# Kernel tuning notes

Hardware: AMD Instinct MI355X
Metric: run time of the kernel (lower is better)

Reference implementation:

```python
import jax, jax.numpy as jnp
import numpy as np
import math

HIDDEN = 2048
HEADS = 16
HEAD_DIM = HIDDEN // HEADS
RANK = HIDDEN // 2  # rank_ratio=0.5
B, S = 1, 4096


def setup_inputs() -> dict:
    key = jax.random.key(0)
    ks = jax.random.split(key, 10)
    sd = lambda fan_in: 1.0 / math.sqrt(fan_in)
    inp = {
        "hidden_states": jax.random.normal(ks[0], (B, S, HIDDEN), dtype=jnp.float32),
        "attention_mask": jnp.zeros((B, 1, S, S), dtype=jnp.float32),
        # low-rank projection weights; Linear weight shape is [out, in]
        "q_V": jax.random.uniform(ks[1], (RANK, HIDDEN), jnp.float32, -sd(HIDDEN), sd(HIDDEN)),
        "q_U": jax.random.uniform(ks[2], (HIDDEN, RANK), jnp.float32, -sd(RANK), sd(RANK)),
        "k_V": jax.random.uniform(ks[3], (RANK, HIDDEN), jnp.float32, -sd(HIDDEN), sd(HIDDEN)),
        "k_U": jax.random.uniform(ks[4], (HIDDEN, RANK), jnp.float32, -sd(RANK), sd(RANK)),
        "v_V": jax.random.uniform(ks[5], (RANK, HIDDEN), jnp.float32, -sd(HIDDEN), sd(HIDDEN)),
        "v_U": jax.random.uniform(ks[6], (HIDDEN, RANK), jnp.float32, -sd(RANK), sd(RANK)),
        "o_W": jax.random.uniform(ks[7], (HIDDEN, HIDDEN), jnp.float32, -sd(HIDDEN), sd(HIDDEN)),
        "o_b": jax.random.uniform(ks[8], (HIDDEN,), jnp.float32, -sd(HIDDEN), sd(HIDDEN)),
    }
    return inp


def _split_heads(x):
    # [B,S,HIDDEN] -> [B,H,S,Dh]
    b, s, _ = x.shape
    return x.reshape(b, s, HEADS, HEAD_DIM).transpose(0, 2, 1, 3)


def reference(hidden_states, attention_mask, q_V, q_U, k_V, k_U, v_V, v_U, o_W, o_b):
    # low-rank QKV: x @ V^T @ U^T
    q = _split_heads((hidden_states @ q_V.T) @ q_U.T)
    k = _split_heads((hidden_states @ k_V.T) @ k_U.T)
    v = _split_heads((hidden_states @ v_V.T) @ v_U.T)
    scores = jnp.einsum("bhqd,bhkd->bhqk", q, k) / math.sqrt(HEAD_DIM)
    scores = scores + attention_mask
    attn = jax.nn.softmax(scores, axis=-1)
    out = jnp.einsum("bhqk,bhkd->bhqd", attn, v)
    out = out.transpose(0, 2, 1, 3).reshape(hidden_states.shape[0], hidden_states.shape[1], HIDDEN)
    out = out @ o_W.T + o_b
    return out
```

## Files before the change

kernel.cpp:

```cpp
#include <hip/hip_runtime.h>

#define HIDDEN 2048
#define HEADS 16
#define HD 128
#define RANK 1024
#define SEQ 4096

typedef __bf16 bf16_t;
typedef __bf16 bf16x8 __attribute__((ext_vector_type(8)));
typedef __bf16 bf16x4 __attribute__((ext_vector_type(4)));
typedef float f32x4 __attribute__((ext_vector_type(4)));

#define MFMA_BF16(a, b, c) __builtin_amdgcn_mfma_f32_16x16x32_bf16((a), (b), (c), 0, 0, 0)

__device__ __forceinline__ void gload16(const bf16_t* g, bf16_t* l) {
  __builtin_amdgcn_global_load_lds(
      (const __attribute__((address_space(1))) unsigned int*)g,
      (__attribute__((address_space(3))) unsigned int*)l, 16, 0, 0);
}

struct CastSeg { const float* s; bf16_t* d; int n4; };
struct CastArgs { CastSeg seg[8]; };

__global__ __launch_bounds__(256) void cast_bf16_kernel(CastArgs a) {
  const int stride = gridDim.x * blockDim.x;
  const int tid0 = blockIdx.x * blockDim.x + threadIdx.x;
#pragma unroll
  for (int i = 0; i < 8; i++) {
    const float4* src = (const float4*)a.seg[i].s;
    bf16x4* dst = (bf16x4*)a.seg[i].d;
    const int n4 = a.seg[i].n4;
    for (int j = tid0; j < n4; j += stride) {
      float4 v = src[j];
      dst[j] = bf16x4{(bf16_t)v.x, (bf16_t)v.y, (bf16_t)v.z, (bf16_t)v.w};
    }
  }
}

template <int OUT_MODE>
__global__ __launch_bounds__(256) void gemm3(const bf16_t* __restrict__ A, int lda, int aOff,
                                             const bf16_t* __restrict__ W0,
                                             const bf16_t* __restrict__ W1,
                                             const bf16_t* __restrict__ W2,
                                             int nPerThird, int K,
                                             void* __restrict__ Cp, int ldc, size_t cOff,
                                             const float* __restrict__ bias, float s0,
                                             bf16_t* __restrict__ Ct) {
  __shared__ bf16_t As[128 * 32];
  __shared__ bf16_t Bs[128 * 32];
  const int tid = threadIdx.x, lane = tid & 63, wave = tid >> 6;
  const int wr = wave >> 1, wc = wave & 1, quad = lane >> 4, l15 = lane & 15;
  const int n0g = blockIdx.x * 128;
  const int third = n0g / nPerThird;
  const int n0 = n0g - third * nPerThird;
  const bf16_t* W = third == 0 ? W0 : (third == 1 ? W1 : W2);
  const bf16_t* Ab = A + (size_t)third * aOff;
  const int m0 = blockIdx.y * 128;
  const float sc = (third == 0) ? s0 : 1.f;

  f32x4 acc[4][4];
#pragma unroll
  for (int i = 0; i < 4; i++)
#pragma unroll
    for (int j = 0; j < 4; j++) acc[i][j] = f32x4{0.f, 0.f, 0.f, 0.f};

  const int KT = K >> 5;
  for (int kt = 0; kt < KT; ++kt) {
#pragma unroll
    for (int i = 0; i < 2; i++) {
      int slot = (wave * 2 + i) * 64 + lane;
      int row = slot >> 2, cp = slot & 3;
      int cl = cp ^ ((row >> 1) & 3);
      gload16(Ab + (size_t)(m0 + row) * lda + kt * 32 + cl * 8, As + (size_t)(wave * 2 + i) * 512);
    }
#pragma unroll
    for (int i = 0; i < 2; i++) {
      int slot = (wave * 2 + i) * 64 + lane;
      int row = slot >> 2, cp = slot & 3;
      int cl = cp ^ ((row >> 1) & 3);
      gload16(W + (size_t)(n0 + row) * K + kt * 32 + cl * 8, Bs + (size_t)(wave * 2 + i) * 512);
    }
    __syncthreads();

    bf16x8 af[4], bfr[4];
#pragma unroll
    for (int mt = 0; mt < 4; mt++) {
      int row = wr * 64 + mt * 16 + l15;
      int phys = quad ^ ((row >> 1) & 3);
      af[mt] = *reinterpret_cast<const bf16x8*>(As + row * 32 + phys * 8);
    }
#pragma unroll
    for (int nt = 0; nt < 4; nt++) {
      int row = wc * 64 + nt * 16 + l15;
      int phys = quad ^ ((row >> 1) & 3);
      bfr[nt] = *reinterpret_cast<const bf16x8*>(Bs + row * 32 + phys * 8);
    }
#pragma unroll
    for (int mt = 0; mt < 4; mt++)
#pragma unroll
      for (int nt = 0; nt < 4; nt++) acc[mt][nt] = MFMA_BF16(af[mt], bfr[nt], acc[mt][nt]);
    __syncthreads();
  }

  if constexpr (OUT_MODE == 2) {
    if (third == 2) {
#pragma unroll
      for (int nt = 0; nt < 4; nt++) {
        int col = n0 + wc * 64 + nt * 16 + l15;
#pragma unroll
        for (int mt = 0; mt < 4; mt++) {
          int rowb = m0 + wr * 64 + mt * 16 + quad * 4;
          bf16x4 tv = {(bf16_t)acc[mt][nt][0], (bf16_t)acc[mt][nt][1],
                       (bf16_t)acc[mt][nt][2], (bf16_t)acc[mt][nt][3]};
          *reinterpret_cast<bf16x4*>(Ct + (size_t)col * SEQ + rowb) = tv;
        }
      }
      return;
    }
  }

#pragma unroll
  for (int nt = 0; nt < 4; nt++) {
    int col = n0 + wc * 64 + nt * 16 + l15;
    float bv = 0.f;
    if constexpr (OUT_MODE == 1) bv = bias[col];
#pragma unroll
    for (int mt = 0; mt < 4; mt++) {
      int rowb = m0 + wr * 64 + mt * 16 + quad * 4;
#pragma unroll
      for (int r = 0; r < 4; r++) {
        float vx = acc[mt][nt][r];
        if constexpr (OUT_MODE == 1)
          ((float*)Cp + (size_t)third * cOff)[(size_t)(rowb + r) * ldc + col] = vx + bv;
        else
          ((bf16_t*)Cp + (size_t)third * cOff)[(size_t)(rowb + r) * ldc + col] = (bf16_t)(vx * sc);
      }
    }
  }
}

__global__ __launch_bounds__(256, 2) void attn_kernel(const bf16_t* __restrict__ qb,
                                                      const bf16_t* __restrict__ kb,
                                                      const bf16_t* __restrict__ vtp,
                                                      const float* __restrict__ mask,
                                                      bf16_t* __restrict__ ao) {
  __shared__ bf16_t Ks[2][64 * 128];
  __shared__ bf16_t Vs[3][128 * 64];
  const int tid = threadIdx.x, lane = tid & 63, w = tid >> 6;
  const int quad = lane >> 4, l15 = lane & 15;
  const int head = blockIdx.x, q0 = blockIdx.y * 128;
  const float LOG2E = 1.4426950408889634f;
  const int NT = SEQ / 64;

  bf16x8 qf[2][4];
#pragma unroll
  for (int qt = 0; qt < 2; qt++)
#pragma unroll
    for (int ks = 0; ks < 4; ks++)
      qf[qt][ks] = *reinterpret_cast<const bf16x8*>(
          qb + (size_t)(q0 + w * 32 + qt * 16 + l15) * HIDDEN + head * HD + ks * 32 + quad * 8);

  f32x4 O[8][2];
#pragma unroll
  for (int dt = 0; dt < 8; dt++)
#pragma unroll
    for (int qt = 0; qt < 2; qt++) O[dt][qt] = f32x4{0.f, 0.f, 0.f, 0.f};
  float lacc[2] = {0.f, 0.f};

  auto stageK = [&](int kt, int buf) {
#pragma unroll
    for (int i = 0; i < 4; i++) {
      int slot = (w * 4 + i) * 64 + lane;
      int row = slot >> 4, cp = slot & 15;
      int cl = cp ^ ((row & 3) | ((row & 8) >> 1));
      gload16(kb + (size_t)(kt * 64 + row) * HIDDEN + head * HD + cl * 8,
              &Ks[buf][(size_t)(w * 4 + i) * 512]);
    }
  };
  auto stageV = [&](int kt, int buf) {
#pragma unroll
    for (int i = 0; i < 4; i++) {
      int slot = (w * 4 + i) * 64 + lane;
      int row = slot >> 3, cp = slot & 7;
      int cl = cp ^ (row & 7);
      gload16(vtp + (size_t)(head * HD + row) * SEQ + kt * 64 + cl * 8,
              &Vs[buf][(size_t)(w * 4 + i) * 512]);
    }
  };

  const int sK = (l15 & 3) | (((l15 >> 2) & 1) << 2);
  const int rA0 = ((l15 >> 2) << 3) + (l15 & 3);

  f32x4 mv[2][2][2];
  auto loadMask = [&](int kt) {
#pragma unroll
    for (int kp = 0; kp < 2; kp++)
#pragma unroll
      for (int sub = 0; sub < 2; sub++)
#pragma unroll
        for (int qt = 0; qt < 2; qt++)
          mv[kp][sub][qt] = *reinterpret_cast<const f32x4*>(
              mask + (size_t)(q0 + w * 32 + qt * 16 + l15) * SEQ + kt * 64 + kp * 32 + quad * 8 +
              sub * 4);
  };

  f32x4 sacc[2][2][2];
  bf16x8 pf[2][2];

  auto smGroup = [&](int kp, int sub) {
#pragma unroll
    for (int qt = 0; qt < 2; qt++) {
      f32x4 e;
#pragma unroll
      for (int r = 0; r < 4; r++)
        e[r] = __builtin_amdgcn_exp2f(sacc[kp][sub][qt][r] + mv[kp][sub][qt][r] * LOG2E);
      lacc[qt] += (e[0] + e[1]) + (e[2] + e[3]);
#pragma unroll
      for (int r = 0; r < 4; r++) pf[kp][qt][sub * 4 + r] = (bf16_t)e[r];
    }
  };

  auto qkT = [&](int buf) {
#pragma unroll
    for (int kp = 0; kp < 2; kp++)
#pragma unroll
      for (int sub = 0; sub < 2; sub++)
#pragma unroll
        for (int qt = 0; qt < 2; qt++) sacc[kp][sub][qt] = f32x4{0.f, 0.f, 0.f, 0.f};
#pragma unroll
    for (int ks = 0; ks < 4; ks++) {
      int phys = (ks * 4 + quad) ^ sK;
#pragma unroll
      for (int kp = 0; kp < 2; kp++)
#pragma unroll
        for (int sub = 0; sub < 2; sub++) {
          int rowA = kp * 32 + sub * 4 + rA0;
          bf16x8 ak = *reinterpret_cast<const bf16x8*>(&Ks[buf][rowA * 128 + phys * 8]);
#pragma unroll
          for (int qt = 0; qt < 2; qt++)
            sacc[kp][sub][qt] = MFMA_BF16(ak, qf[qt][ks], sacc[kp][sub][qt]);
        }
    }
  };

  auto qkT_sm = [&](int buf) {
    f32x4 ns[2][2][2];
#pragma unroll
    for (int kp = 0; kp < 2; kp++)
#pragma unroll
      for (int sub = 0; sub < 2; sub++)
#pragma unroll
        for (int qt = 0; qt < 2; qt++) ns[kp][sub][qt] = f32x4{0.f, 0.f, 0.f, 0.f};
#pragma unroll
    for (int ks = 0; ks < 4; ks++) {
      int phys = (ks * 4 + quad) ^ sK;
#pragma unroll
      for (int kp = 0; kp < 2; kp++)
#pragma unroll
        for (int sub = 0; sub < 2; sub++) {
          int rowA = kp * 32 + sub * 4 + rA0;
          bf16x8 ak = *reinterpret_cast<const bf16x8*>(&Ks[buf][rowA * 128 + phys * 8]);
#pragma unroll
          for (int qt = 0; qt < 2; qt++)
            ns[kp][sub][qt] = MFMA_BF16(ak, qf[qt][ks], ns[kp][sub][qt]);
        }
      smGroup(ks >> 1, ks & 1);
    }
#pragma unroll
    for (int kp = 0; kp < 2; kp++)
#pragma unroll
      for (int sub = 0; sub < 2; sub++)
#pragma unroll
        for (int qt = 0; qt < 2; qt++) sacc[kp][sub][qt] = ns[kp][sub][qt];
  };

  auto pv = [&](const bf16_t* Vb) {
#pragma unroll
    for (int kp = 0; kp < 2; kp++)
#pragma unroll
      for (int dt = 0; dt < 8; dt++) {
        int row = dt * 16 + l15;
        int phys = (kp * 4 + quad) ^ (l15 & 7);
        bf16x8 av = *reinterpret_cast<const bf16x8*>(&Vb[row * 64 + phys * 8]);
#pragma unroll
        for (int qt = 0; qt < 2; qt++) O[dt][qt] = MFMA_BF16(av, pf[kp][qt], O[dt][qt]);
      }
  };

  stageK(0, 0);
  stageV(0, 0);
  stageK(1, 1);
  stageV(1, 1);
  loadMask(0);
  __syncthreads();
  qkT(0);

  int vb_pv = 0;
  int vb_st = 2;
  for (int t = 0; t < NT - 1; ++t) {
    __syncthreads();
    stageK(t + 2, t & 1);
    stageV(t + 2, vb_st);
    __builtin_amdgcn_s_setprio(1);
    qkT_sm((t + 1) & 1);
    __builtin_amdgcn_s_setprio(0);
    loadMask(t + 1);
    __builtin_amdgcn_s_setprio(1);
    pv(&Vs[vb_pv][0]);
    __builtin_amdgcn_s_setprio(0);
    vb_pv = vb_pv == 2 ? 0 : vb_pv + 1;
    vb_st = vb_st == 2 ? 0 : vb_st + 1;
  }
  smGroup(0, 0);
  smGroup(0, 1);
  smGroup(1, 0);
  smGroup(1, 1);
  pv(&Vs[vb_pv][0]);

#pragma unroll
  for (int qt = 0; qt < 2; qt++) {
    float l = lacc[qt];
    l += __shfl_xor(l, 16, 64);
    l += __shfl_xor(l, 32, 64);
    lacc[qt] = 1.f / l;
  }
#pragma unroll
  for (int dt = 0; dt < 8; dt++)
#pragma unroll
    for (int qt = 0; qt < 2; qt++) {
      int q = q0 + w * 32 + qt * 16 + l15;
      int d = head * HD + dt * 16 + quad * 4;
      f32x4 o = O[dt][qt];
      bf16x4 ov = {(bf16_t)(o[0] * lacc[qt]), (bf16_t)(o[1] * lacc[qt]),
                   (bf16_t)(o[2] * lacc[qt]), (bf16_t)(o[3] * lacc[qt])};
      *reinterpret_cast<bf16x4*>(ao + (size_t)q * HIDDEN + d) = ov;
    }
}

extern "C" void kernel_launch(void* const* d_in, const int* in_sizes, int n_in,
                              void* d_out, int out_size, void* d_ws, size_t ws_size,
                              hipStream_t stream) {
  (void)in_sizes; (void)n_in; (void)out_size; (void)ws_size;
  const float* x = (const float*)d_in[0];
  const float* mask = (const float*)d_in[1];
  const float* qV = (const float*)d_in[2];
  const float* qU = (const float*)d_in[3];
  const float* kV = (const float*)d_in[4];
  const float* kU = (const float*)d_in[5];
  const float* vV = (const float*)d_in[6];
  const float* vU = (const float*)d_in[7];
  const float* oW = (const float*)d_in[8];
  const float* ob = (const float*)d_in[9];
  float* out = (float*)d_out;

  char* ws = (char*)d_ws;
  const size_t MB = 1ull << 20;
  bf16_t* xb  = (bf16_t*)(ws);
  bf16_t* tmp = (bf16_t*)(ws + 16 * MB);
  bf16_t* qkv = (bf16_t*)(ws + 40 * MB);
  bf16_t* qVb = (bf16_t*)(ws + 88 * MB);
  bf16_t* qUb = (bf16_t*)(ws + 92 * MB);
  bf16_t* kVb = (bf16_t*)(ws + 96 * MB);
  bf16_t* kUb = (bf16_t*)(ws + 100 * MB);
  bf16_t* vVb = (bf16_t*)(ws + 104 * MB);
  bf16_t* vUb = (bf16_t*)(ws + 108 * MB);
  bf16_t* oWb = (bf16_t*)(ws + 112 * MB);
  bf16_t* vt = qkv + 2 * (size_t)SEQ * HIDDEN;

  const float kQScale = 0.088388347648318447f * 1.4426950408889634f;

  CastArgs ca;
  ca.seg[0] = {x, xb, SEQ * HIDDEN / 4};
  ca.seg[1] = {qV, qVb, RANK * HIDDEN / 4};
  ca.seg[2] = {qU, qUb, HIDDEN * RANK / 4};
  ca.seg[3] = {kV, kVb, RANK * HIDDEN / 4};
  ca.seg[4] = {kU, kUb, HIDDEN * RANK / 4};
  ca.seg[5] = {vV, vVb, RANK * HIDDEN / 4};
  ca.seg[6] = {vU, vUb, HIDDEN * RANK / 4};
  ca.seg[7] = {oW, oWb, HIDDEN * HIDDEN / 4};
  cast_bf16_kernel<<<2048, 256, 0, stream>>>(ca);

  gemm3<0><<<dim3(24, 32), 256, 0, stream>>>(xb, HIDDEN, 0, qVb, kVb, vVb, RANK, HIDDEN,
                                             tmp, 3 * RANK, (size_t)RANK, nullptr, 1.f, nullptr);
  gemm3<2><<<dim3(48, 32), 256, 0, stream>>>(tmp, 3 * RANK, RANK, qUb, kUb, vUb, HIDDEN, RANK,
                                             qkv, HIDDEN, (size_t)SEQ * HIDDEN, nullptr,
                                             kQScale, vt);
  attn_kernel<<<dim3(HEADS, SEQ / 128), 256, 0, stream>>>(qkv, qkv + (size_t)SEQ * HIDDEN, vt,
                                                          mask, xb);
  gemm3<1><<<dim3(16, 32), 256, 0, stream>>>(xb, HIDDEN, 0, oWb, oWb, oWb, HIDDEN, HIDDEN,
                                             out, HIDDEN, 0, ob, 1.f, nullptr);
}
```

Measured before the change: 558.3 us.

## Use 8 waves per attention block with 16 query rows each

```diff
diff --git a/kernel.cpp b/kernel.cpp
--- a/kernel.cpp
+++ b/kernel.cpp
@@ -139,7 +139,7 @@
   }
 }
 
-__global__ __launch_bounds__(256, 2) void attn_kernel(const bf16_t* __restrict__ qb,
+__global__ __launch_bounds__(512, 2) void attn_kernel(const bf16_t* __restrict__ qb,
                                                       const bf16_t* __restrict__ kb,
                                                       const bf16_t* __restrict__ vtp,
                                                       const float* __restrict__ mask,
@@ -149,84 +149,73 @@
   const int tid = threadIdx.x, lane = tid & 63, w = tid >> 6;
   const int quad = lane >> 4, l15 = lane & 15;
   const int head = blockIdx.x, q0 = blockIdx.y * 128;
+  const int qrow = q0 + w * 16 + l15;
   const float LOG2E = 1.4426950408889634f;
   const int NT = SEQ / 64;
 
-  bf16x8 qf[2][4];
-#pragma unroll
-  for (int qt = 0; qt < 2; qt++)
-#pragma unroll
-    for (int ks = 0; ks < 4; ks++)
-      qf[qt][ks] = *reinterpret_cast<const bf16x8*>(
-          qb + (size_t)(q0 + w * 32 + qt * 16 + l15) * HIDDEN + head * HD + ks * 32 + quad * 8);
-
-  f32x4 O[8][2];
-#pragma unroll
-  for (int dt = 0; dt < 8; dt++)
-#pragma unroll
-    for (int qt = 0; qt < 2; qt++) O[dt][qt] = f32x4{0.f, 0.f, 0.f, 0.f};
-  float lacc[2] = {0.f, 0.f};
+  bf16x8 qf[4];
+#pragma unroll
+  for (int ks = 0; ks < 4; ks++)
+    qf[ks] = *reinterpret_cast<const bf16x8*>(qb + (size_t)qrow * HIDDEN + head * HD + ks * 32 +
+                                              quad * 8);
+
+  f32x4 O[8];
+#pragma unroll
+  for (int dt = 0; dt < 8; dt++) O[dt] = f32x4{0.f, 0.f, 0.f, 0.f};
+  float lacc = 0.f;
 
   auto stageK = [&](int kt, int buf) {
 #pragma unroll
-    for (int i = 0; i < 4; i++) {
-      int slot = (w * 4 + i) * 64 + lane;
+    for (int i = 0; i < 2; i++) {
+      int slot = (w * 2 + i) * 64 + lane;
       int row = slot >> 4, cp = slot & 15;
       int cl = cp ^ ((row & 3) | ((row & 8) >> 1));
       gload16(kb + (size_t)(kt * 64 + row) * HIDDEN + head * HD + cl * 8,
-              &Ks[buf][(size_t)(w * 4 + i) * 512]);
+              &Ks[buf][(size_t)(w * 2 + i) * 512]);
     }
   };
   auto stageV = [&](int kt, int buf) {
 #pragma unroll
-    for (int i = 0; i < 4; i++) {
-      int slot = (w * 4 + i) * 64 + lane;
+    for (int i = 0; i < 2; i++) {
+      int slot = (w * 2 + i) * 64 + lane;
       int row = slot >> 3, cp = slot & 7;
       int cl = cp ^ (row & 7);
       gload16(vtp + (size_t)(head * HD + row) * SEQ + kt * 64 + cl * 8,
-              &Vs[buf][(size_t)(w * 4 + i) * 512]);
+              &Vs[buf][(size_t)(w * 2 + i) * 512]);
     }
   };
 
   const int sK = (l15 & 3) | (((l15 >> 2) & 1) << 2);
   const int rA0 = ((l15 >> 2) << 3) + (l15 & 3);
 
-  f32x4 mv[2][2][2];
+  f32x4 mv[2][2];
   auto loadMask = [&](int kt) {
 #pragma unroll
     for (int kp = 0; kp < 2; kp++)
 #pragma unroll
       for (int sub = 0; sub < 2; sub++)
-#pragma unroll
-        for (int qt = 0; qt < 2; qt++)
-          mv[kp][sub][qt] = *reinterpret_cast<const f32x4*>(
-              mask + (size_t)(q0 + w * 32 + qt * 16 + l15) * SEQ + kt * 64 + kp * 32 + quad * 8 +
-              sub * 4);
-  };
-
-  f32x4 sacc[2][2][2];
-  bf16x8 pf[2][2];
+        mv[kp][sub] = *reinterpret_cast<const f32x4*>(
+            mask + (size_t)qrow * SEQ + kt * 64 + kp * 32 + quad * 8 + sub * 4);
+  };
+
+  f32x4 sacc[2][2];
+  bf16x8 pf[2];
 
   auto smGroup = [&](int kp, int sub) {
-#pragma unroll
-    for (int qt = 0; qt < 2; qt++) {
-      f32x4 e;
-#pragma unroll
-      for (int r = 0; r < 4; r++)
-        e[r] = __builtin_amdgcn_exp2f(sacc[kp][sub][qt][r] + mv[kp][sub][qt][r] * LOG2E);
-      lacc[qt] += (e[0] + e[1]) + (e[2] + e[3]);
-#pragma unroll
-      for (int r = 0; r < 4; r++) pf[kp][qt][sub * 4 + r] = (bf16_t)e[r];
-    }
+    f32x4 e;
+#pragma unroll
+    for (int r = 0; r < 4; r++)
+      e[r] = __builtin_amdgcn_exp2f(sacc[kp][sub][r] + mv[kp][sub][r] * LOG2E);
+    lacc += (e[0] + e[1]) + (e[2] + e[3]);
+#pragma unroll
+    for (int r = 0; r < 4; r++) pf[kp][sub * 4 + r] = (bf16_t)e[r];
   };
 
   auto qkT = [&](int buf) {
 #pragma unroll
     for (int kp = 0; kp < 2; kp++)
 #pragma unroll
-      for (int sub = 0; sub < 2; sub++)
-#pragma unroll
-        for (int qt = 0; qt < 2; qt++) sacc[kp][sub][qt] = f32x4{0.f, 0.f, 0.f, 0.f};
+      for (int sub = 0; sub < 2; sub++) sacc[kp][sub] = f32x4{0.f, 0.f, 0.f, 0.f};
 #pragma unroll
     for (int ks = 0; ks < 4; ks++) {
       int phys = (ks * 4 + quad) ^ sK;
@@ -236,21 +225,17 @@
         for (int sub = 0; sub < 2; sub++) {
           int rowA = kp * 32 + sub * 4 + rA0;
           bf16x8 ak = *reinterpret_cast<const bf16x8*>(&Ks[buf][rowA * 128 + phys * 8]);
-#pragma unroll
-          for (int qt = 0; qt < 2; qt++)
-            sacc[kp][sub][qt] = MFMA_BF16(ak, qf[qt][ks], sacc[kp][sub][qt]);
+          sacc[kp][sub] = MFMA_BF16(ak, qf[ks], sacc[kp][sub]);
         }
     }
   };
 
   auto qkT_sm = [&](int buf) {
-    f32x4 ns[2][2][2];
-#pragma unroll
-    for (int kp = 0; kp < 2; kp++)
-#pragma unroll
-      for (int sub = 0; sub < 2; sub++)
-#pragma unroll
-        for (int qt = 0; qt < 2; qt++) ns[kp][sub][qt] = f32x4{0.f, 0.f, 0.f, 0.f};
+    f32x4 ns[2][2];
+#pragma unroll
+    for (int kp = 0; kp < 2; kp++)
+#pragma unroll
+      for (int sub = 0; sub < 2; sub++) ns[kp][sub] = f32x4{0.f, 0.f, 0.f, 0.f};
 #pragma unroll
     for (int ks = 0; ks < 4; ks++) {
       int phys = (ks * 4 + quad) ^ sK;
@@ -260,18 +245,14 @@
         for (int sub = 0; sub < 2; sub++) {
           int rowA = kp * 32 + sub * 4 + rA0;
           bf16x8 ak = *reinterpret_cast<const bf16x8*>(&Ks[buf][rowA * 128 + phys * 8]);
-#pragma unroll
-          for (int qt = 0; qt < 2; qt++)
-            ns[kp][sub][qt] = MFMA_BF16(ak, qf[qt][ks], ns[kp][sub][qt]);
+          ns[kp][sub] = MFMA_BF16(ak, qf[ks], ns[kp][sub]);
         }
       smGroup(ks >> 1, ks & 1);
     }
 #pragma unroll
     for (int kp = 0; kp < 2; kp++)
 #pragma unroll
-      for (int sub = 0; sub < 2; sub++)
-#pragma unroll
-        for (int qt = 0; qt < 2; qt++) sacc[kp][sub][qt] = ns[kp][sub][qt];
+      for (int sub = 0; sub < 2; sub++) sacc[kp][sub] = ns[kp][sub];
   };
 
   auto pv = [&](const bf16_t* Vb) {
@@ -282,8 +263,7 @@
         int row = dt * 16 + l15;
         int phys = (kp * 4 + quad) ^ (l15 & 7);
         bf16x8 av = *reinterpret_cast<const bf16x8*>(&Vb[row * 64 + phys * 8]);
-#pragma unroll
-        for (int qt = 0; qt < 2; qt++) O[dt][qt] = MFMA_BF16(av, pf[kp][qt], O[dt][qt]);
+        O[dt] = MFMA_BF16(av, pf[kp], O[dt]);
       }
   };
 
@@ -317,24 +297,20 @@
   smGroup(1, 1);
   pv(&Vs[vb_pv][0]);
 
-#pragma unroll
-  for (int qt = 0; qt < 2; qt++) {
-    float l = lacc[qt];
+  {
+    float l = lacc;
     l += __shfl_xor(l, 16, 64);
     l += __shfl_xor(l, 32, 64);
-    lacc[qt] = 1.f / l;
-  }
-#pragma unroll
-  for (int dt = 0; dt < 8; dt++)
-#pragma unroll
-    for (int qt = 0; qt < 2; qt++) {
-      int q = q0 + w * 32 + qt * 16 + l15;
-      int d = head * HD + dt * 16 + quad * 4;
-      f32x4 o = O[dt][qt];
-      bf16x4 ov = {(bf16_t)(o[0] * lacc[qt]), (bf16_t)(o[1] * lacc[qt]),
-                   (bf16_t)(o[2] * lacc[qt]), (bf16_t)(o[3] * lacc[qt])};
-      *reinterpret_cast<bf16x4*>(ao + (size_t)q * HIDDEN + d) = ov;
-    }
+    lacc = 1.f / l;
+  }
+#pragma unroll
+  for (int dt = 0; dt < 8; dt++) {
+    int d = head * HD + dt * 16 + quad * 4;
+    f32x4 o = O[dt];
+    bf16x4 ov = {(bf16_t)(o[0] * lacc), (bf16_t)(o[1] * lacc),
+                 (bf16_t)(o[2] * lacc), (bf16_t)(o[3] * lacc)};
+    *reinterpret_cast<bf16x4*>(ao + (size_t)qrow * HIDDEN + d) = ov;
+  }
 }
 
 extern "C" void kernel_launch(void* const* d_in, const int* in_sizes, int n_in,
@@ -385,7 +361,7 @@
   gemm3<2><<<dim3(48, 32), 256, 0, stream>>>(tmp, 3 * RANK, RANK, qUb, kUb, vUb, HIDDEN, RANK,
                                              qkv, HIDDEN, (size_t)SEQ * HIDDEN, nullptr,
                                              kQScale, vt);
-  attn_kernel<<<dim3(HEADS, SEQ / 128), 256, 0, stream>>>(qkv, qkv + (size_t)SEQ * HIDDEN, vt,
+  attn_kernel<<<dim3(HEADS, SEQ / 128), 512, 0, stream>>>(qkv, qkv + (size_t)SEQ * HIDDEN, vt,
                                                           mask, xb);
   gemm3<1><<<dim3(16, 32), 256, 0, stream>>>(xb, HIDDEN, 0, oWb, oWb, oWb, HIDDEN, HIDDEN,
                                              out, HIDDEN, 0, ob, 1.f, nullptr);
```

After: 616.6 us. 10.4% more time.
